# Kernel tuning notes

Hardware: AMD Instinct MI355X
Metric: run time of the kernel (lower is better)

The kernel has to match this reference:

```python
import jax, jax.numpy as jnp
import numpy as np

B, S, D_IN, D_OUT = 2, 2048, 4096, 4096


def setup_inputs() -> dict:
    key = jax.random.key(0)
    kx, kw, kb = jax.random.split(key, 3)
    x = jax.random.normal(kx, (B, S, D_IN), dtype=jnp.float32)
    weight = jax.random.normal(kw, (D_OUT, D_IN), dtype=jnp.float32)
    bias = jax.random.normal(kb, (D_OUT,), dtype=jnp.float32)
    return {"x": x, "weight": weight, "bias": bias}


def reference(x, weight, bias):
    # FdaBinary forward is simply sign(); linear with binarized weight.
    w_bin = jnp.sign(weight)  # [D_OUT, D_IN], values in {-1, 0, +1}
    # F.linear: x @ w.T + b
    out = jnp.einsum("bsd,od->bso", x, w_bin) + bias
    return out
```

## Files before the change

### kernel.cpp

```cpp
#include <hip/hip_runtime.h>
#include <hip/hip_bf16.h>
#include <stdint.h>
#include <stddef.h>

#define M_DIM 4096
#define N_DIM 4096
#define K_DIM 4096

#define BM 128
#define BN 128
#define BK 32

typedef __bf16 bf16;
typedef __attribute__((ext_vector_type(4))) __bf16 bf16x4;
typedef __attribute__((ext_vector_type(8))) __bf16 bf16x8;
typedef __attribute__((ext_vector_type(4))) float f32x4;

__global__ void prep_kernel(const float* __restrict__ x, const float* __restrict__ w,
                            bf16* __restrict__ xb, bf16* __restrict__ wb, int nv ) {
    int stride = gridDim.x * blockDim.x;
    for (int idx = blockIdx.x * blockDim.x + threadIdx.x; idx < nv; idx += stride) {
        float4 xv = ((const float4*)x)[idx];
        bf16x4 xo;
        xo[0] = (bf16)xv.x; xo[1] = (bf16)xv.y; xo[2] = (bf16)xv.z; xo[3] = (bf16)xv.w;
        ((bf16x4*)xb)[idx] = xo;

        float4 wv = ((const float4*)w)[idx];
        bf16x4 wo;
        wo[0] = (bf16)((wv.x > 0.f) ? 1.f : ((wv.x < 0.f) ? -1.f : 0.f));
        wo[1] = (bf16)((wv.y > 0.f) ? 1.f : ((wv.y < 0.f) ? -1.f : 0.f));
        wo[2] = (bf16)((wv.z > 0.f) ? 1.f : ((wv.z < 0.f) ? -1.f : 0.f));
        wo[3] = (bf16)((wv.w > 0.f) ? 1.f : ((wv.w < 0.f) ? -1.f : 0.f));
        ((bf16x4*)wb)[idx] = wo;
    }
}

__device__ __forceinline__ void load_lds16(const void* g, void* l) {
    __builtin_amdgcn_global_load_lds(
        (const __attribute__((address_space(1))) void*)g,
        (__attribute__((address_space(3))) void*)l, 16, 0, 0);
}

__global__ __launch_bounds__(256) void gemm_bin_kernel(const bf16* __restrict__ A,
                                                       const bf16* __restrict__ Bw,
                                                       const float* __restrict__ bias,
                                                       float* __restrict__ C) {
    __shared__ __align__(16) bf16 As[BM * BK];
    __shared__ __align__(16) bf16 Bs[BN * BK];

    const int tid  = threadIdx.x;
    const int lane = tid & 63;
    const int wave = tid >> 6;
    const int wm   = wave & 1;
    const int wn   = wave >> 1;

    const int tileM = blockIdx.y * BM;
    const int tileN = blockIdx.x * BN;

    const int c0 = wave;
    const int c1 = wave + 4;
    const int rowInC = lane >> 2;
    const int colE   = (lane & 3) * 8;

    const bf16* gA0 = A  + (size_t)(tileM + c0 * 16 + rowInC) * K_DIM + colE;
    const bf16* gA1 = A  + (size_t)(tileM + c1 * 16 + rowInC) * K_DIM + colE;
    const bf16* gB0 = Bw + (size_t)(tileN + c0 * 16 + rowInC) * K_DIM + colE;
    const bf16* gB1 = Bw + (size_t)(tileN + c1 * 16 + rowInC) * K_DIM + colE;

    bf16* lA0 = As + c0 * 512;
    bf16* lA1 = As + c1 * 512;
    bf16* lB0 = Bs + c0 * 512;
    bf16* lB1 = Bs + c1 * 512;

    f32x4 acc[4][4];
#pragma unroll
    for (int i = 0; i < 4; ++i)
#pragma unroll
        for (int j = 0; j < 4; ++j)
            acc[i][j] = (f32x4){0.f, 0.f, 0.f, 0.f};

    const int fragRowA = wm * 64 + (lane & 15);
    const int fragRowB = wn * 64 + (lane & 15);
    const int fragK    = (lane >> 4) * 8;

    const int nK = K_DIM / BK;
    for (int kt = 0; kt < nK; ++kt) {
        load_lds16(gA0, lA0);
        load_lds16(gA1, lA1);
        load_lds16(gB0, lB0);
        load_lds16(gB1, lB1);
        gA0 += BK; gA1 += BK; gB0 += BK; gB1 += BK;

        __syncthreads();

        bf16x8 af[4], bfr[4];
#pragma unroll
        for (int i = 0; i < 4; ++i)
            af[i] = *(const bf16x8*)&As[(fragRowA + i * 16) * BK + fragK];
#pragma unroll
        for (int j = 0; j < 4; ++j)
            bfr[j] = *(const bf16x8*)&Bs[(fragRowB + j * 16) * BK + fragK];

#pragma unroll
        for (int i = 0; i < 4; ++i)
#pragma unroll
            for (int j = 0; j < 4; ++j)
                acc[i][j] = __builtin_amdgcn_mfma_f32_16x16x32_bf16(af[i], bfr[j], acc[i][j], 0, 0, 0);

        __syncthreads();
    }

#pragma unroll
    for (int j = 0; j < 4; ++j) {
        const int col = tileN + wn * 64 + j * 16 + (lane & 15);
        const float bv = bias[col];
#pragma unroll
        for (int i = 0; i < 4; ++i) {
            const int row0 = tileM + wm * 64 + i * 16 + ((lane >> 4) << 2);
#pragma unroll
            for (int r = 0; r < 4; ++r) {
                C[(size_t)(row0 + r) * N_DIM + col] = acc[i][j][r] + bv;
            }
        }
    }
}

extern "C" void kernel_launch(void* const* d_in, const int* in_sizes, int n_in,
                              void* d_out, int out_size, void* d_ws, size_t ws_size,
                              hipStream_t stream) {
    const float* x    = (const float*)d_in[0];
    const float* w    = (const float*)d_in[1];
    const float* bias = (const float*)d_in[2];
    float* out        = (float*)d_out;

    const int nElem = M_DIM * K_DIM;
    bf16* xb = (bf16*)d_ws;
    bf16* wb = xb + (size_t)nElem;

    prep_kernel<<<4096, 256, 0, stream>>>(x, w, xb, wb, nElem / 4);

    dim3 grid(N_DIM / BN, M_DIM / BM);
    gemm_bin_kernel<<<grid, 256, 0, stream>>>(xb, wb, bias, out);
}
```

Measured before the change: 346.6 us.

## Double-buffer LDS tiles, swizzle LDS layout, group tiles for L2, flatten prep grid

The GEMM kernel now double-buffers its LDS tiles, issuing the next K-slice's global-to-LDS loads before computing on the current one, and drops one of the two barriers per iteration. An XOR swizzle on the 16-byte chunk index is applied consistently to the load source and the fragment reads to reduce LDS bank conflicts. Tiles are remapped through a 1D grid into 16x16 super-tiles to improve L2 reuse. The prep kernel launches one thread per vector instead of using a grid-stride loop. Double buffering doubles LDS use per block, which may lower occupancy, and the single barrier relies on the async loads being ordered correctly.

```diff
diff --git a/kernel.cpp b/kernel.cpp
--- a/kernel.cpp
+++ b/kernel.cpp
@@ -6,33 +6,33 @@
 #define M_DIM 4096
 #define N_DIM 4096
 #define K_DIM 4096
-
 #define BM 128
 #define BN 128
 #define BK 32
+#define NKT (K_DIM / BK)
 
 typedef __bf16 bf16;
 typedef __attribute__((ext_vector_type(4))) __bf16 bf16x4;
 typedef __attribute__((ext_vector_type(8))) __bf16 bf16x8;
 typedef __attribute__((ext_vector_type(4))) float f32x4;
 
-__global__ void prep_kernel(const float* __restrict__ x, const float* __restrict__ w,
-                            bf16* __restrict__ xb, bf16* __restrict__ wb, int nv ) {
-    int stride = gridDim.x * blockDim.x;
-    for (int idx = blockIdx.x * blockDim.x + threadIdx.x; idx < nv; idx += stride) {
-        float4 xv = ((const float4*)x)[idx];
-        bf16x4 xo;
-        xo[0] = (bf16)xv.x; xo[1] = (bf16)xv.y; xo[2] = (bf16)xv.z; xo[3] = (bf16)xv.w;
-        ((bf16x4*)xb)[idx] = xo;
+__global__ __launch_bounds__(256) void prep_kernel(const float* __restrict__ x,
+                                                   const float* __restrict__ w,
+                                                   bf16* __restrict__ xb,
+                                                   bf16* __restrict__ wb) {
+    const int idx = blockIdx.x * 256 + threadIdx.x;
+    float4 xv = ((const float4*)x)[idx];
+    bf16x4 xo;
+    xo[0] = (bf16)xv.x; xo[1] = (bf16)xv.y; xo[2] = (bf16)xv.z; xo[3] = (bf16)xv.w;
+    ((bf16x4*)xb)[idx] = xo;
 
-        float4 wv = ((const float4*)w)[idx];
-        bf16x4 wo;
-        wo[0] = (bf16)((wv.x > 0.f) ? 1.f : ((wv.x < 0.f) ? -1.f : 0.f));
-        wo[1] = (bf16)((wv.y > 0.f) ? 1.f : ((wv.y < 0.f) ? -1.f : 0.f));
-        wo[2] = (bf16)((wv.z > 0.f) ? 1.f : ((wv.z < 0.f) ? -1.f : 0.f));
-        wo[3] = (bf16)((wv.w > 0.f) ? 1.f : ((wv.w < 0.f) ? -1.f : 0.f));
-        ((bf16x4*)wb)[idx] = wo;
-    }
+    float4 wv = ((const float4*)w)[idx];
+    bf16x4 wo;
+    wo[0] = (bf16)((wv.x > 0.f) ? 1.f : ((wv.x < 0.f) ? -1.f : 0.f));
+    wo[1] = (bf16)((wv.y > 0.f) ? 1.f : ((wv.y < 0.f) ? -1.f : 0.f));
+    wo[2] = (bf16)((wv.z > 0.f) ? 1.f : ((wv.z < 0.f) ? -1.f : 0.f));
+    wo[3] = (bf16)((wv.w > 0.f) ? 1.f : ((wv.w < 0.f) ? -1.f : 0.f));
+    ((bf16x4*)wb)[idx] = wo;
 }
 
 __device__ __forceinline__ void load_lds16(const void* g, void* l) {
@@ -45,8 +45,8 @@
                                                        const bf16* __restrict__ Bw,
                                                        const float* __restrict__ bias,
                                                        float* __restrict__ C) {
-    __shared__ __align__(16) bf16 As[BM * BK];
-    __shared__ __align__(16) bf16 Bs[BN * BK];
+    __shared__ __align__(16) bf16 As[2][BM * BK];
+    __shared__ __align__(16) bf16 Bs[2][BN * BK];
 
     const int tid  = threadIdx.x;
     const int lane = tid & 63;
@@ -54,23 +54,22 @@
     const int wm   = wave & 1;
     const int wn   = wave >> 1;
 
-    const int tileM = blockIdx.y * BM;
-    const int tileN = blockIdx.x * BN;
+    const int pid  = blockIdx.x;
+    const int supm = (pid >> 8) & 1;
+    const int supn = pid >> 9;
+    const int r    = pid & 255;
+    const int tileM = (supm * 16 + (r >> 4)) * BM;
+    const int tileN = (supn * 16 + (r & 15)) * BN;
 
+    const int rowInC = lane >> 2;
+    const int q_src  = (lane & 3) ^ ((lane >> 3) & 3);
     const int c0 = wave;
     const int c1 = wave + 4;
-    const int rowInC = lane >> 2;
-    const int colE   = (lane & 3) * 8;
 
-    const bf16* gA0 = A  + (size_t)(tileM + c0 * 16 + rowInC) * K_DIM + colE;
-    const bf16* gA1 = A  + (size_t)(tileM + c1 * 16 + rowInC) * K_DIM + colE;
-    const bf16* gB0 = Bw + (size_t)(tileN + c0 * 16 + rowInC) * K_DIM + colE;
-    const bf16* gB1 = Bw + (size_t)(tileN + c1 * 16 + rowInC) * K_DIM + colE;
-
-    bf16* lA0 = As + c0 * 512;
-    bf16* lA1 = As + c1 * 512;
-    bf16* lB0 = Bs + c0 * 512;
-    bf16* lB1 = Bs + c1 * 512;
+    const bf16* gA0 = A  + (size_t)(tileM + c0 * 16 + rowInC) * K_DIM + q_src * 8;
+    const bf16* gA1 = A  + (size_t)(tileM + c1 * 16 + rowInC) * K_DIM + q_src * 8;
+    const bf16* gB0 = Bw + (size_t)(tileN + c0 * 16 + rowInC) * K_DIM + q_src * 8;
+    const bf16* gB1 = Bw + (size_t)(tileN + c1 * 16 + rowInC) * K_DIM + q_src * 8;
 
     f32x4 acc[4][4];
 #pragma unroll
@@ -79,47 +78,56 @@
         for (int j = 0; j < 4; ++j)
             acc[i][j] = (f32x4){0.f, 0.f, 0.f, 0.f};
 
-    const int fragRowA = wm * 64 + (lane & 15);
-    const int fragRowB = wn * 64 + (lane & 15);
-    const int fragK    = (lane >> 4) * 8;
+    const int l15 = lane & 15;
+    const int qf  = lane >> 4;
+    const int slt = qf ^ ((l15 >> 1) & 3);
+    const int fragRowA = wm * 64 + l15;
+    const int fragRowB = wn * 64 + l15;
+    const int fragOff  = slt * 8;
 
-    const int nK = K_DIM / BK;
-    for (int kt = 0; kt < nK; ++kt) {
-        load_lds16(gA0, lA0);
-        load_lds16(gA1, lA1);
-        load_lds16(gB0, lB0);
-        load_lds16(gB1, lB1);
-        gA0 += BK; gA1 += BK; gB0 += BK; gB1 += BK;
+    load_lds16(gA0, &As[0][c0 * 512]);
+    load_lds16(gA1, &As[0][c1 * 512]);
+    load_lds16(gB0, &Bs[0][c0 * 512]);
+    load_lds16(gB1, &Bs[0][c1 * 512]);
 
+    for (int kt = 0; kt < NKT; ++kt) {
+        const int cur = kt & 1;
         __syncthreads();
+
+        if (kt + 1 < NKT) {
+            const int nxt  = cur ^ 1;
+            const size_t ko = (size_t)(kt + 1) * BK;
+            load_lds16(gA0 + ko, &As[nxt][c0 * 512]);
+            load_lds16(gA1 + ko, &As[nxt][c1 * 512]);
+            load_lds16(gB0 + ko, &Bs[nxt][c0 * 512]);
+            load_lds16(gB1 + ko, &Bs[nxt][c1 * 512]);
+        }
 
         bf16x8 af[4], bfr[4];
 #pragma unroll
         for (int i = 0; i < 4; ++i)
-            af[i] = *(const bf16x8*)&As[(fragRowA + i * 16) * BK + fragK];
+            af[i] = *(const bf16x8*)&As[cur][(fragRowA + i * 16) * BK + fragOff];
 #pragma unroll
         for (int j = 0; j < 4; ++j)
-            bfr[j] = *(const bf16x8*)&Bs[(fragRowB + j * 16) * BK + fragK];
+            bfr[j] = *(const bf16x8*)&Bs[cur][(fragRowB + j * 16) * BK + fragOff];
 
 #pragma unroll
         for (int i = 0; i < 4; ++i)
 #pragma unroll
             for (int j = 0; j < 4; ++j)
                 acc[i][j] = __builtin_amdgcn_mfma_f32_16x16x32_bf16(af[i], bfr[j], acc[i][j], 0, 0, 0);
-
-        __syncthreads();
     }
 
 #pragma unroll
     for (int j = 0; j < 4; ++j) {
-        const int col = tileN + wn * 64 + j * 16 + (lane & 15);
+        const int col = tileN + wn * 64 + j * 16 + l15;
         const float bv = bias[col];
 #pragma unroll
         for (int i = 0; i < 4; ++i) {
-            const int row0 = tileM + wm * 64 + i * 16 + ((lane >> 4) << 2);
+            const int row0 = tileM + wm * 64 + i * 16 + (qf << 2);
 #pragma unroll
-            for (int r = 0; r < 4; ++r) {
-                C[(size_t)(row0 + r) * N_DIM + col] = acc[i][j][r] + bv;
+            for (int rr = 0; rr < 4; ++rr) {
+                C[(size_t)(row0 + rr) * N_DIM + col] = acc[i][j][rr] + bv;
             }
         }
     }
@@ -137,8 +145,7 @@
     bf16* xb = (bf16*)d_ws;
     bf16* wb = xb + (size_t)nElem;
 
-    prep_kernel<<<4096, 256, 0, stream>>>(x, w, xb, wb, nElem / 4);
+    prep_kernel<<<nElem / 4 / 256, 256, 0, stream>>>(x, w, xb, wb);
 
-    dim3 grid(N_DIM / BN, M_DIM / BM);
-    gemm_bin_kernel<<<grid, 256, 0, stream>>>(xb, wb, bias, out);
+    gemm_bin_kernel<<<(M_DIM / BM) * (N_DIM / BN), 256, 0, stream>>>(xb, wb, bias, out);
 }
```

Result: slower. 372.5 us (+7.5%).
